# Kernel tuning notes

Measured on AMD Instinct MI355X. Metric: run time of the kernel, lower is better.

The kernel has to match this reference:

```python
import jax, jax.numpy as jnp
import numpy as np

CHUNK = 32
PRIOR = 64
POSE = 512
PRED = 128
B = 2048


def setup_inputs() -> dict:
    key = jax.random.key(0)
    k1, k2, k3, k4, k5, k6 = jax.random.split(key, 6)
    initial_feature = jax.random.normal(k1, (B, PRIOR, POSE), dtype=jnp.float32)
    pred_feature = jax.random.normal(k2, (B, PRED, POSE), dtype=jnp.float32)
    s1 = 1.0 / np.sqrt(CHUNK * POSE)
    s2 = 1.0 / np.sqrt(POSE)
    W1 = jax.random.uniform(k3, (POSE, CHUNK * POSE), minval=-s1, maxval=s1, dtype=jnp.float32)
    b1 = jax.random.uniform(k4, (POSE,), minval=-s1, maxval=s1, dtype=jnp.float32)
    W2 = jax.random.uniform(k5, (POSE, POSE), minval=-s2, maxval=s2, dtype=jnp.float32)
    b2 = jax.random.uniform(k6, (POSE,), minval=-s2, maxval=s2, dtype=jnp.float32)
    return {"initial_feature": initial_feature, "pred_feature": pred_feature,
            "W1": W1, "b1": b1, "W2": W2, "b2": b2}


def reference(initial_feature, pred_feature, W1, b1, W2, b2):
    Bn = initial_feature.shape[0]
    # last CHUNK prior frames flattened -> [B, CHUNK*POSE]
    x = initial_feature[:, PRIOR - CHUNK:, :].reshape(Bn, -1)
    # spatial_chunk_encoder (Dropout is identity in eval mode)
    mem = (x @ W1.T + b1) @ W2.T + b2          # [B, POSE]
    head = pred_feature[:, :CHUNK, :]          # [B, CHUNK, POSE]
    score = jnp.einsum('bd,bcd->bc', mem, head)  # per-token dot product
    g = jax.nn.sigmoid(score)[..., None]       # [B, CHUNK, 1]
    blended = g * head + (1.0 - g) * mem[:, None, :]
    return pred_feature.at[:, :CHUNK, :].set(blended)
```

## Files before the change

### kernel.cpp

```cpp
#include <hip/hip_runtime.h>
#include <hip/hip_bf16.h>
#include <stdint.h>

#define CHUNKC 32
#define PRIORC 64
#define POSEC 512
#define PREDC 128
#define NB 2048
#define K1 (CHUNKC*POSEC)
#define KS 8
#define KCH (K1/KS)

typedef __attribute__((ext_vector_type(8))) short bf16x8;
typedef __attribute__((ext_vector_type(4))) float f32x4;

__device__ __forceinline__ unsigned short f2b(float f) {
    union { float f; unsigned int u; } x; x.f = f;
    unsigned int r = x.u + 0x7fffu + ((x.u >> 16) & 1u);
    return (unsigned short)(r >> 16);
}

__device__ __forceinline__ void gload_lds16(const void* g, void* l) {
    __builtin_amdgcn_global_load_lds(
        (const __attribute__((address_space(1))) unsigned int*)g,
        (__attribute__((address_space(3))) unsigned int*)l, 16, 0, 0);
}

#define XN4   8388608
#define W1N4  2097152
#define W2N4  65536
__global__ __launch_bounds__(256) void cvt_all_kernel(const float4* __restrict__ init,
                                                      const float4* __restrict__ W1,
                                                      const float4* __restrict__ W2,
                                                      ushort4* __restrict__ xb,
                                                      ushort4* __restrict__ w1b,
                                                      ushort4* __restrict__ w2b) {
    const int64_t n = XN4 + W1N4 + W2N4;
    const int64_t stride = (int64_t)gridDim.x * blockDim.x;
    for (int64_t i = (int64_t)blockIdx.x * blockDim.x + threadIdx.x; i < n; i += stride) {
        float4 v; ushort4* dst;
        if (i < XN4) {
            int64_t b = i >> 12, r = i & 4095;
            v = init[b * 8192 + 4096 + r];
            dst = xb + i;
        } else if (i < XN4 + W1N4) {
            v = W1[i - XN4];
            dst = w1b + (i - XN4);
        } else {
            v = W2[i - XN4 - W1N4];
            dst = w2b + (i - XN4 - W1N4);
        }
        *dst = make_ushort4(f2b(v.x), f2b(v.y), f2b(v.z), f2b(v.w));
    }
}

__global__ __launch_bounds__(256) void gemm1_copy_kernel(const ushort* __restrict__ xb,
                                                         const ushort* __restrict__ w1b,
                                                         float* __restrict__ part,
                                                         const float4* __restrict__ pred4,
                                                         float4* __restrict__ out4) {
    __shared__ ushort As[128][64];
    __shared__ ushort Bs[128][64];
    const int t = threadIdx.x;
    const int bid = blockIdx.x;

    if (bid >= 512) {
        const int cid = bid - 512;
        const int b = cid >> 1, h = cid & 1;
        const int64_t base = (int64_t)b * 16384 + 4096 + h * 6144;
#pragma unroll
        for (int i = 0; i < 24; ++i) {
            int64_t idx = base + i * 256 + t;
            out4[idx] = pred4[idx];
        }
        return;
    }

    const int l = t & 63, wid = t >> 6;
    const int wr = wid >> 1, wc = wid & 1;
    const int mt = bid & 15, nt = (bid >> 4) & 3, ks = bid >> 6;

    f32x4 acc[4][4] = {};

    const ushort* aG = xb  + (int64_t)(mt * 128) * K1 + ks * KCH;
    const ushort* bG = w1b + (int64_t)(nt * 128) * K1 + ks * KCH;
    const int srow = t >> 3, scol = (t & 7) * 8;

    const int fr = l & 15, fq = l >> 4;

    for (int k0 = 0; k0 < KCH; k0 += 64) {
#pragma unroll
        for (int i = 0; i < 4; ++i) {
            gload_lds16(aG + (int64_t)(i * 32 + srow) * K1 + k0 + scol,
                        (char*)&As[0][0] + i * 4096 + wid * 1024);
            gload_lds16(bG + (int64_t)(i * 32 + srow) * K1 + k0 + scol,
                        (char*)&Bs[0][0] + i * 4096 + wid * 1024);
        }
        __syncthreads();
#pragma unroll
        for (int k2 = 0; k2 < 2; ++k2) {
            bf16x8 a[4], b[4];
#pragma unroll
            for (int m = 0; m < 4; ++m)
                a[m] = *(const bf16x8*)&As[wr * 64 + m * 16 + fr][k2 * 32 + fq * 8];
#pragma unroll
            for (int n = 0; n < 4; ++n)
                b[n] = *(const bf16x8*)&Bs[wc * 64 + n * 16 + fr][k2 * 32 + fq * 8];
#pragma unroll
            for (int m = 0; m < 4; ++m)
#pragma unroll
                for (int n = 0; n < 4; ++n)
                    acc[m][n] = __builtin_amdgcn_mfma_f32_16x16x32_bf16(a[m], b[n], acc[m][n], 0, 0, 0);
        }
        __syncthreads();
    }

    float* P = part + (int64_t)ks * NB * POSEC;
    const int mbase = mt * 128 + wr * 64, nbase = nt * 128 + wc * 64;
#pragma unroll
    for (int m = 0; m < 4; ++m)
#pragma unroll
        for (int n = 0; n < 4; ++n) {
            int row0 = mbase + m * 16 + fq * 4;
            int col  = nbase + n * 16 + fr;
#pragma unroll
            for (int r = 0; r < 4; ++r)
                P[(int64_t)(row0 + r) * POSEC + col] = acc[m][n][r];
        }
}

__global__ __launch_bounds__(256) void reduce_kernel(const float4* __restrict__ part,
                                                     const float* __restrict__ b1,
                                                     ushort4* __restrict__ A2) {
    const int i4 = blockIdx.x * 256 + threadIdx.x;
    float4 s = part[i4];
#pragma unroll
    for (int k = 1; k < KS; ++k) {
        float4 p = part[(int64_t)k * 262144 + i4];
        s.x += p.x; s.y += p.y; s.z += p.z; s.w += p.w;
    }
    const int col = (i4 * 4) & 511;
    float4 bv = *(const float4*)&b1[col];
    A2[i4] = make_ushort4(f2b(s.x + bv.x), f2b(s.y + bv.y), f2b(s.z + bv.z), f2b(s.w + bv.w));
}

__global__ __launch_bounds__(256) void gemm2_kernel(const ushort* __restrict__ A2,
                                                    const ushort* __restrict__ w2b,
                                                    const float* __restrict__ b2,
                                                    float* __restrict__ mem) {
    __shared__ ushort As[64][64];
    __shared__ ushort Bs[64][64];
    const int t = threadIdx.x;
    const int l = t & 63, wid = t >> 6;
    const int wr = wid >> 1, wc = wid & 1;
    const int mt = blockIdx.x >> 3, nt = blockIdx.x & 7;

    f32x4 acc[2][2] = {};
    const ushort* aG = A2  + (int64_t)(mt * 64) * POSEC;
    const ushort* bG = w2b + (int64_t)(nt * 64) * POSEC;
    const int srow = t >> 3, scol = (t & 7) * 8;
    const int fr = l & 15, fq = l >> 4;

    for (int k0 = 0; k0 < POSEC; k0 += 64) {
#pragma unroll
        for (int i = 0; i < 2; ++i) {
            gload_lds16(aG + (int64_t)(i * 32 + srow) * POSEC + k0 + scol,
                        (char*)&As[0][0] + i * 4096 + wid * 1024);
            gload_lds16(bG + (int64_t)(i * 32 + srow) * POSEC + k0 + scol,
                        (char*)&Bs[0][0] + i * 4096 + wid * 1024);
        }
        __syncthreads();
#pragma unroll
        for (int k2 = 0; k2 < 2; ++k2) {
            bf16x8 a[2], b[2];
#pragma unroll
            for (int m = 0; m < 2; ++m)
                a[m] = *(const bf16x8*)&As[wr * 32 + m * 16 + fr][k2 * 32 + fq * 8];
#pragma unroll
            for (int n = 0; n < 2; ++n)
                b[n] = *(const bf16x8*)&Bs[wc * 32 + n * 16 + fr][k2 * 32 + fq * 8];
#pragma unroll
            for (int m = 0; m < 2; ++m)
#pragma unroll
                for (int n = 0; n < 2; ++n)
                    acc[m][n] = __builtin_amdgcn_mfma_f32_16x16x32_bf16(a[m], b[n], acc[m][n], 0, 0, 0);
        }
        __syncthreads();
    }

    const int mbase = mt * 64 + wr * 32, nbase = nt * 64 + wc * 32;
#pragma unroll
    for (int m = 0; m < 2; ++m)
#pragma unroll
        for (int n = 0; n < 2; ++n) {
            int row0 = mbase + m * 16 + fq * 4;
            int col  = nbase + n * 16 + fr;
            float bias = b2[col];
#pragma unroll
            for (int r = 0; r < 4; ++r)
                mem[(int64_t)(row0 + r) * POSEC + col] = acc[m][n][r] + bias;
        }
}

__global__ __launch_bounds__(256) void blend_head_kernel(const float* __restrict__ pred,
                                                         const float* __restrict__ mem,
                                                         float* __restrict__ out) {
    const int b = blockIdx.x;
    const int t = threadIdx.x;
    __shared__ float sm[POSEC];
    __shared__ float sg[CHUNKC];

    sm[t]       = mem[(int64_t)b * POSEC + t];
    sm[t + 256] = mem[(int64_t)b * POSEC + 256 + t];
    __syncthreads();

    const int l = t & 63, wid = t >> 6;
    const float4* sm4 = (const float4*)sm;
    const float4* p4 = (const float4*)pred + (int64_t)b * 16384;
    float4* o4 = (float4*)out + (int64_t)b * 16384;

#pragma unroll
    for (int ci = 0; ci < 8; ++ci) {
        int c = wid * 8 + ci;
        float4 h0 = p4[c * 128 + l * 2];
        float4 h1 = p4[c * 128 + l * 2 + 1];
        float4 m0 = sm4[l * 2];
        float4 m1 = sm4[l * 2 + 1];
        float s = h0.x * m0.x + h0.y * m0.y + h0.z * m0.z + h0.w * m0.w
                + h1.x * m1.x + h1.y * m1.y + h1.z * m1.z + h1.w * m1.w;
#pragma unroll
        for (int o = 32; o; o >>= 1) s += __shfl_xor(s, o);
        if (l == 0) sg[c] = 1.0f / (1.0f + expf(-s));
    }
    __syncthreads();

#pragma unroll
    for (int i = 0; i < 16; ++i) {
        int idx = i * 256 + t;
        int row = idx >> 7, c4 = idx & 127;
        float g = sg[row];
        float4 h = p4[idx];
        float4 m = sm4[c4];
        float4 r;
        r.x = g * h.x + (1.0f - g) * m.x;
        r.y = g * h.y + (1.0f - g) * m.y;
        r.z = g * h.z + (1.0f - g) * m.z;
        r.w = g * h.w + (1.0f - g) * m.w;
        o4[idx] = r;
    }
}


extern "C" void kernel_launch(void* const* d_in, const int* in_sizes, int n_in,
                              void* d_out, int out_size, void* d_ws, size_t ws_size,
                              hipStream_t stream) {
    const float* init = (const float*)d_in[0];
    const float* pred = (const float*)d_in[1];
    const float* W1   = (const float*)d_in[2];
    const float* b1   = (const float*)d_in[3];
    const float* W2   = (const float*)d_in[4];
    const float* b2   = (const float*)d_in[5];
    float* out = (float*)d_out;

    char* ws = (char*)d_ws;
    ushort* xb   = (ushort*)(ws);
    ushort* w1b  = (ushort*)(ws + 67108864);
    ushort* w2b  = (ushort*)(ws + 83886080);
    float*  part = (float*) (ws + 84410368);
    ushort* A2   = (ushort*)(ws + 117964800);
    float*  mem  = (float*) (ws + 120061952);

    cvt_all_kernel<<<2560, 256, 0, stream>>>((const float4*)init, (const float4*)W1,
                                             (const float4*)W2,
                                             (ushort4*)xb, (ushort4*)w1b, (ushort4*)w2b);
    gemm1_copy_kernel<<<512 + 4096, 256, 0, stream>>>(xb, w1b, part,
                                                      (const float4*)pred, (float4*)out);
    reduce_kernel<<<1024, 256, 0, stream>>>((const float4*)part, b1, (ushort4*)A2);
    gemm2_kernel<<<256, 256, 0, stream>>>(A2, w2b, b2, mem);
    blend_head_kernel<<<NB, 256, 0, stream>>>(pred, mem, out);
}
```

Baseline: 352.9 us.

## Shrink GEMM1 M-tile, remap blocks for L2 locality, move tail copy into blend

GEMM1 now uses 64x128 tiles with 1024 blocks instead of 128x128 with 512, raising block count and occupancy (launch bounds 256,4). Block indices are permuted so that neighbouring blocks land on different XCDs and blocks sharing a K-slice group together. The untouched tail copy of pred_feature is taken out of the GEMM1 launch and done at the end of the blend kernel, one block per batch. The costs are lower per-tile reuse in GEMM1 and a longer serial blend kernel in place of a copy that previously overlapped with the GEMM.

```diff
diff --git a/kernel.cpp b/kernel.cpp
--- a/kernel.cpp
+++ b/kernel.cpp
@@ -54,35 +54,20 @@
     }
 }
 
-__global__ __launch_bounds__(256) void gemm1_copy_kernel(const ushort* __restrict__ xb,
-                                                         const ushort* __restrict__ w1b,
-                                                         float* __restrict__ part,
-                                                         const float4* __restrict__ pred4,
-                                                         float4* __restrict__ out4) {
-    __shared__ ushort As[128][64];
+__global__ __launch_bounds__(256, 4) void gemm1_kernel(const ushort* __restrict__ xb,
+                                                       const ushort* __restrict__ w1b,
+                                                       float* __restrict__ part) {
+    __shared__ ushort As[64][64];
     __shared__ ushort Bs[128][64];
     const int t = threadIdx.x;
-    const int bid = blockIdx.x;
-
-    if (bid >= 512) {
-        const int cid = bid - 512;
-        const int b = cid >> 1, h = cid & 1;
-        const int64_t base = (int64_t)b * 16384 + 4096 + h * 6144;
-#pragma unroll
-        for (int i = 0; i < 24; ++i) {
-            int64_t idx = base + i * 256 + t;
-            out4[idx] = pred4[idx];
-        }
-        return;
-    }
-
     const int l = t & 63, wid = t >> 6;
     const int wr = wid >> 1, wc = wid & 1;
-    const int mt = bid & 15, nt = (bid >> 4) & 3, ks = bid >> 6;
-
-    f32x4 acc[4][4] = {};
-
-    const ushort* aG = xb  + (int64_t)(mt * 128) * K1 + ks * KCH;
+    const int orig = (blockIdx.x & 7) * 128 + (blockIdx.x >> 3);
+    const int mt = orig & 31, nt = (orig >> 5) & 3, ks = orig >> 7;
+
+    f32x4 acc[2][4] = {};
+
+    const ushort* aG = xb  + (int64_t)(mt * 64)  * K1 + ks * KCH;
     const ushort* bG = w1b + (int64_t)(nt * 128) * K1 + ks * KCH;
     const int srow = t >> 3, scol = (t & 7) * 8;
 
@@ -90,24 +75,25 @@
 
     for (int k0 = 0; k0 < KCH; k0 += 64) {
 #pragma unroll
-        for (int i = 0; i < 4; ++i) {
+        for (int i = 0; i < 2; ++i)
             gload_lds16(aG + (int64_t)(i * 32 + srow) * K1 + k0 + scol,
                         (char*)&As[0][0] + i * 4096 + wid * 1024);
+#pragma unroll
+        for (int i = 0; i < 4; ++i)
             gload_lds16(bG + (int64_t)(i * 32 + srow) * K1 + k0 + scol,
                         (char*)&Bs[0][0] + i * 4096 + wid * 1024);
-        }
         __syncthreads();
 #pragma unroll
         for (int k2 = 0; k2 < 2; ++k2) {
-            bf16x8 a[4], b[4];
-#pragma unroll
-            for (int m = 0; m < 4; ++m)
-                a[m] = *(const bf16x8*)&As[wr * 64 + m * 16 + fr][k2 * 32 + fq * 8];
+            bf16x8 a[2], b[4];
+#pragma unroll
+            for (int m = 0; m < 2; ++m)
+                a[m] = *(const bf16x8*)&As[wr * 32 + m * 16 + fr][k2 * 32 + fq * 8];
 #pragma unroll
             for (int n = 0; n < 4; ++n)
                 b[n] = *(const bf16x8*)&Bs[wc * 64 + n * 16 + fr][k2 * 32 + fq * 8];
 #pragma unroll
-            for (int m = 0; m < 4; ++m)
+            for (int m = 0; m < 2; ++m)
 #pragma unroll
                 for (int n = 0; n < 4; ++n)
                     acc[m][n] = __builtin_amdgcn_mfma_f32_16x16x32_bf16(a[m], b[n], acc[m][n], 0, 0, 0);
@@ -116,9 +102,9 @@
     }
 
     float* P = part + (int64_t)ks * NB * POSEC;
-    const int mbase = mt * 128 + wr * 64, nbase = nt * 128 + wc * 64;
-#pragma unroll
-    for (int m = 0; m < 4; ++m)
+    const int mbase = mt * 64 + wr * 32, nbase = nt * 128 + wc * 64;
+#pragma unroll
+    for (int m = 0; m < 2; ++m)
 #pragma unroll
         for (int n = 0; n < 4; ++n) {
             int row0 = mbase + m * 16 + fq * 4;
@@ -202,9 +188,9 @@
         }
 }
 
-__global__ __launch_bounds__(256) void blend_head_kernel(const float* __restrict__ pred,
-                                                         const float* __restrict__ mem,
-                                                         float* __restrict__ out) {
+__global__ __launch_bounds__(256) void blend_kernel(const float* __restrict__ pred,
+                                                    const float* __restrict__ mem,
+                                                    float* __restrict__ out) {
     const int b = blockIdx.x;
     const int t = threadIdx.x;
     __shared__ float sm[POSEC];
@@ -248,6 +234,11 @@
         r.w = g * h.w + (1.0f - g) * m.w;
         o4[idx] = r;
     }
+#pragma unroll
+    for (int i = 0; i < 48; ++i) {
+        int idx = 4096 + i * 256 + t;
+        o4[idx] = p4[idx];
+    }
 }
 
 
@@ -273,9 +264,8 @@
     cvt_all_kernel<<<2560, 256, 0, stream>>>((const float4*)init, (const float4*)W1,
                                              (const float4*)W2,
                                              (ushort4*)xb, (ushort4*)w1b, (ushort4*)w2b);
-    gemm1_copy_kernel<<<512 + 4096, 256, 0, stream>>>(xb, w1b, part,
-                                                      (const float4*)pred, (float4*)out);
+    gemm1_kernel<<<1024, 256, 0, stream>>>(xb, w1b, part);
     reduce_kernel<<<1024, 256, 0, stream>>>((const float4*)part, b1, (ushort4*)A2);
     gemm2_kernel<<<256, 256, 0, stream>>>(A2, w2b, b2, mem);
-    blend_head_kernel<<<NB, 256, 0, stream>>>(pred, mem, out);
-}
+    blend_kernel<<<NB, 256, 0, stream>>>(pred, mem, out);
+}
```

Result: faster. 345.9 us (-2.0%).
